# Performance work log

Hardware: AMD Instinct MI355X
Metric: run time of the kernel (lower is better)

The kernel has to match this reference:

```python
import jax, jax.numpy as jnp
import numpy as np
import math

D_MODEL = 1024
N_HEAD = 16
D_K = D_MODEL // N_HEAD  # 64
SEQ = 1024
BATCH = 8


def setup_inputs() -> dict:
    k = jax.random.key(0)
    ks = jax.random.split(k, 11)
    f32 = jnp.float32
    scale = 1.0 / math.sqrt(D_MODEL)
    return {
        "query": jax.random.normal(ks[0], (BATCH, SEQ, D_MODEL), dtype=f32),
        "key": jax.random.normal(ks[1], (BATCH, SEQ, D_MODEL), dtype=f32),
        "value": jax.random.normal(ks[2], (BATCH, SEQ, D_MODEL), dtype=f32),
        # Shaw-style relative position table a[q_pos, k_pos, d_k]
        "rel": jax.random.normal(ks[3], (SEQ, SEQ, D_K), dtype=f32) * 0.02,
        "W_q": jax.random.normal(ks[4], (D_MODEL, D_MODEL), dtype=f32) * scale,
        "b_q": jnp.zeros((D_MODEL,), dtype=f32),
        "W_k": jax.random.normal(ks[5], (D_MODEL, D_MODEL), dtype=f32) * scale,
        "b_k": jnp.zeros((D_MODEL,), dtype=f32),
        "W_v": jax.random.normal(ks[6], (D_MODEL, D_MODEL), dtype=f32) * scale,
        "b_v": jnp.zeros((D_MODEL,), dtype=f32),
        # boolean mask: True = masked out (matches torch masked_fill semantics)
        "mask": jax.random.randint(ks[7], (BATCH, SEQ, SEQ), 0, 4) == 0,
    }


def reference(query, key, value, rel, W_q, b_q, W_k, b_k, W_v, b_v, mask):
    B, S, D = query.shape
    H, dk = N_HEAD, D // N_HEAD

    def proj(x, W, b):
        # [B,S,D] -> [B,H,S,dk]
        return (x @ W + b).reshape(B, S, H, dk).transpose(0, 2, 1, 3)

    Q = proj(query, W_q, b_q)
    K = proj(key, W_k, b_k)
    V = proj(value, W_v, b_v)

    # E_1 = Q K^T / sqrt(d_k): [B,H,Sq,Sk]
    scores = jnp.einsum("bhqd,bhkd->bhqk", Q, K) / math.sqrt(dk)
    # E_2 = Q x relative_position (per query position), added UNscaled as in source
    scores = scores + jnp.einsum("bhqd,qkd->bhqk", Q, rel)
    # masked_fill(mask, -1e8)
    scores = jnp.where(mask[:, None, :, :], jnp.float32(-1e8), scores)
    attn = jax.nn.softmax(scores, axis=-1)
    out = jnp.einsum("bhqk,bhkd->bhqd", attn, V)  # [B,H,S,dk]
    return out.transpose(0, 2, 1, 3).reshape(B, S, D)
```

## Files before the change

kernel.cpp:

```cpp
#include <hip/hip_runtime.h>

typedef _Float16 h8_t __attribute__((ext_vector_type(8)));
typedef _Float16 h4_t __attribute__((ext_vector_type(4)));
typedef float f4_t __attribute__((ext_vector_type(4)));

#define MFMA16(a, b, c) __builtin_amdgcn_mfma_f32_16x16x32_f16((a), (b), (c), 0, 0, 0)

__device__ inline void gl_lds16(const _Float16* g, _Float16* l) {
    __builtin_amdgcn_global_load_lds(
        (const __attribute__((address_space(1))) unsigned int*)g,
        (__attribute__((address_space(3))) unsigned int*)l, 16, 0, 0);
}

__global__ void cvt4(const float* __restrict__ in, _Float16* __restrict__ out, int n4) {
    int i = blockIdx.x * 256 + threadIdx.x;
    if (i < n4) {
        f4_t v = *(const f4_t*)(in + (size_t)i * 4);
        h4_t h;
        for (int j = 0; j < 4; ++j) h[j] = (_Float16)v[j];
        *(h4_t*)(out + (size_t)i * 4) = h;
    }
}

__global__ void wtrans(const float* __restrict__ W, _Float16* __restrict__ Wt) {
    __shared__ float tile[32][33];
    int tid = threadIdx.x;
    int tx = tid & 31, ty = tid >> 5;
    int nb = blockIdx.x * 32, kb = blockIdx.y * 32;
    for (int p = 0; p < 4; ++p)
        tile[ty + p * 8][tx] = W[(size_t)(kb + ty + p * 8) * 1024 + nb + tx];
    __syncthreads();
    for (int p = 0; p < 4; ++p)
        Wt[(size_t)(nb + ty + p * 8) * 1024 + kb + tx] = (_Float16)tile[tx][ty + p * 8];
}

__global__ __launch_bounds__(256, 2) void proj_gemm(
    const _Float16* __restrict__ X, const _Float16* __restrict__ Wt,
    const float* __restrict__ bias, _Float16* __restrict__ Out,
    float scale, int vmode)
{
    __shared__ __align__(16) _Float16 Asm[128 * 32];
    __shared__ __align__(16) _Float16 Bsm[128 * 32];
    int tid = threadIdx.x;
    int wave = tid >> 6, lane = tid & 63;
    int l15 = lane & 15, quad = lane >> 4;
    int m0 = blockIdx.x * 128, n0 = blockIdx.y * 128;
    int wm = (wave >> 1) * 64, wn = (wave & 1) * 64;
    f4_t acc[4][4] = {};
    int f0 = wave * 128 + lane;

    for (int kt = 0; kt < 1024; kt += 32) {
        for (int j = 0; j < 2; ++j) {
            int f = f0 + j * 64;
            int r = f >> 2, c = (f & 3) * 8;
            gl_lds16(&X[(size_t)(m0 + r) * 1024 + kt + c], &Asm[f * 8]);
            gl_lds16(&Wt[(size_t)(n0 + r) * 1024 + kt + c], &Bsm[f * 8]);
        }
        __syncthreads();
        h8_t af[4], bf[4];
        for (int i = 0; i < 4; ++i) af[i] = *(const h8_t*)&Asm[(wm + i * 16 + l15) * 32 + quad * 8];
        for (int j = 0; j < 4; ++j) bf[j] = *(const h8_t*)&Bsm[(wn + j * 16 + l15) * 32 + quad * 8];
        for (int i = 0; i < 4; ++i)
            for (int j = 0; j < 4; ++j)
                acc[i][j] = MFMA16(af[i], bf[j], acc[i][j]);
        __syncthreads();
    }
    for (int j = 0; j < 4; ++j) {
        int n = n0 + wn + j * 16 + l15;
        float bv = bias[n];
        int h = n >> 6, d = n & 63;
        for (int i = 0; i < 4; ++i) {
            for (int r = 0; r < 4; ++r) {
                int m = m0 + wm + i * 16 + quad * 4 + r;
                int bb = m >> 10, ss = m & 1023;
                float v = (acc[i][j][r] + bv) * scale;
                size_t oidx = vmode ? (((size_t)(bb * 16 + h) * 64 + d) * 1024 + ss)
                                    : (((size_t)(bb * 16 + h) * 1024 + ss) * 64 + d);
                Out[oidx] = (_Float16)v;
            }
        }
    }
}

__device__ inline h8_t ld_rel(const _Float16* relh, const float* relf, size_t idx) {
    if (relh) return *(const h8_t*)(relh + idx);
    f4_t a = *(const f4_t*)(relf + idx);
    f4_t b = *(const f4_t*)(relf + idx + 4);
    h8_t h;
    for (int j = 0; j < 4; ++j) { h[j] = (_Float16)a[j]; h[4 + j] = (_Float16)b[j]; }
    return h;
}

__global__ __launch_bounds__(256, 2) void attn_kernel(
    const _Float16* __restrict__ Qh,
    const _Float16* __restrict__ Kh,
    const _Float16* __restrict__ Vt,
    const _Float16* __restrict__ relh,
    const float* __restrict__ relf,
    const int* __restrict__ mask,
    float* __restrict__ out)
{
    __shared__ __align__(16) _Float16 R_lds[2][16][17][36];
    __shared__ __align__(16) _Float16 P_lds[16][16][40];

    const int tid = threadIdx.x;
    const int wave = tid >> 6, lane = tid & 63;
    const int l15 = lane & 15, quad = lane >> 4;
    const int b = blockIdx.y;
    const int q0 = blockIdx.x * 16;

    h8_t bQ[4][2];
    h8_t bR[4][2];
    for (int gi = 0; gi < 4; ++gi) {
        int g = wave * 4 + gi;
        const _Float16* qp = Qh + ((size_t)(b * 16 + g) * 1024 + q0 + l15) * 64 + quad * 8;
        bQ[gi][0] = *(const h8_t*)qp;
        bQ[gi][1] = *(const h8_t*)(qp + 32);
    }
    for (int qi = 0; qi < 4; ++qi) {
        int q = q0 + wave * 4 + qi;
        const _Float16* qp = Qh + ((size_t)(b * 16 + l15) * 1024 + q) * 64 + quad * 8;
        bR[qi][0] = *(const h8_t*)qp;
        bR[qi][1] = *(const h8_t*)(qp + 32);
    }

    f4_t acc[4][4] = {};
    float mst[4], lst[4];
    for (int gi = 0; gi < 4; ++gi) { mst[gi] = -1e30f; lst[gi] = 0.0f; }

    int buf = 0;
    for (int t0 = 0; t0 < 1024; t0 += 32, buf ^= 1) {
        const int* mrow = &mask[((size_t)b * 1024 + q0 + l15) * 1024 + t0];
        int4 mk0 = *(const int4*)(mrow + quad * 4);
        int4 mk1 = *(const int4*)(mrow + 16 + quad * 4);

        h8_t relv[4][2][2];
        for (int qi = 0; qi < 4; ++qi) {
            size_t rb = ((size_t)(q0 + wave * 4 + qi) * 1024 + t0 + l15) * 64 + quad * 8;
            relv[qi][0][0] = ld_rel(relh, relf, rb);
            relv[qi][0][1] = ld_rel(relh, relf, rb + 32);
            relv[qi][1][0] = ld_rel(relh, relf, rb + 1024);
            relv[qi][1][1] = ld_rel(relh, relf, rb + 1056);
        }
        for (int qi = 0; qi < 4; ++qi) {
            for (int tm = 0; tm < 2; ++tm) {
                f4_t c = {0.f, 0.f, 0.f, 0.f};
                c = MFMA16(relv[qi][tm][0], bR[qi][0], c);
                c = MFMA16(relv[qi][tm][1], bR[qi][1], c);
                h4_t h;
                for (int r = 0; r < 4; ++r) h[r] = (_Float16)c[r];
                *(h4_t*)&R_lds[buf][wave * 4 + qi][l15][tm * 16 + quad * 4] = h;
            }
        }

        h8_t kv[4][2][2];
        for (int gi = 0; gi < 4; ++gi) {
            const _Float16* kp =
                Kh + ((size_t)(b * 16 + wave * 4 + gi) * 1024 + t0 + l15) * 64 + quad * 8;
            kv[gi][0][0] = *(const h8_t*)kp;
            kv[gi][0][1] = *(const h8_t*)(kp + 32);
            kv[gi][1][0] = *(const h8_t*)(kp + 1024);
            kv[gi][1][1] = *(const h8_t*)(kp + 1056);
        }
        __syncthreads();

        int mm[8] = {mk0.x, mk0.y, mk0.z, mk0.w, mk1.x, mk1.y, mk1.z, mk1.w};

        for (int gi = 0; gi < 4; ++gi) {
            int g = wave * 4 + gi;
            f4_t s[2];
            for (int tm = 0; tm < 2; ++tm) {
                h4_t rh = *(const h4_t*)&R_lds[buf][l15][g][tm * 16 + quad * 4];
                f4_t c;
                for (int r = 0; r < 4; ++r) c[r] = (float)rh[r];
                c = MFMA16(kv[gi][tm][0], bQ[gi][0], c);
                c = MFMA16(kv[gi][tm][1], bQ[gi][1], c);
                s[tm] = c;
            }
            for (int tm = 0; tm < 2; ++tm)
                for (int r = 0; r < 4; ++r)
                    if (mm[tm * 4 + r]) s[tm][r] = -1e8f;

            float mx = s[0][0];
            for (int tm = 0; tm < 2; ++tm)
                for (int r = 0; r < 4; ++r) mx = fmaxf(mx, s[tm][r]);
            mx = fmaxf(mx, __shfl_xor(mx, 16));
            mx = fmaxf(mx, __shfl_xor(mx, 32));
            float mnew = fmaxf(mst[gi], mx);
            float alpha = __expf(mst[gi] - mnew);
            mst[gi] = mnew;
            float rs = 0.0f;
            for (int tm = 0; tm < 2; ++tm)
                for (int r = 0; r < 4; ++r) {
                    float p = __expf(s[tm][r] - mnew);
                    s[tm][r] = p;
                    rs += p;
                }
            rs += __shfl_xor(rs, 16);
            rs += __shfl_xor(rs, 32);
            lst[gi] = lst[gi] * alpha + rs;
            for (int dm = 0; dm < 4; ++dm) acc[gi][dm] *= alpha;
            for (int tm = 0; tm < 2; ++tm) {
                h4_t h;
                for (int r = 0; r < 4; ++r) h[r] = (_Float16)s[tm][r];
                *(h4_t*)&P_lds[g][l15][tm * 16 + quad * 4] = h;
            }
        }

        h8_t vv[4][4];
        for (int gi = 0; gi < 4; ++gi) {
            const _Float16* vp =
                Vt + (size_t)(b * 16 + wave * 4 + gi) * 65536 + t0 + quad * 8;
            for (int dm = 0; dm < 4; ++dm)
                vv[gi][dm] = *(const h8_t*)(vp + (size_t)(dm * 16 + l15) * 1024);
        }
        for (int gi = 0; gi < 4; ++gi) {
            h8_t bp = *(const h8_t*)&P_lds[wave * 4 + gi][l15][quad * 8];
            for (int dm = 0; dm < 4; ++dm)
                acc[gi][dm] = MFMA16(vv[gi][dm], bp, acc[gi][dm]);
        }
    }

    for (int gi = 0; gi < 4; ++gi) {
        int g = wave * 4 + gi;
        float linv = 1.0f / lst[gi];
        for (int dm = 0; dm < 4; ++dm) {
            f4_t v = acc[gi][dm] * linv;
            float* op = out + ((size_t)b * 1024 + q0 + l15) * 1024 + g * 64 + dm * 16 + quad * 4;
            *(f4_t*)op = v;
        }
    }
}

extern "C" void kernel_launch(void* const* d_in, const int* in_sizes, int n_in,
                              void* d_out, int out_size, void* d_ws, size_t ws_size,
                              hipStream_t stream) {
    const float* q    = (const float*)d_in[0];
    const float* k    = (const float*)d_in[1];
    const float* v    = (const float*)d_in[2];
    const float* rel  = (const float*)d_in[3];
    const float* Wq   = (const float*)d_in[4];
    const float* bq   = (const float*)d_in[5];
    const float* Wk   = (const float*)d_in[6];
    const float* bk   = (const float*)d_in[7];
    const float* Wv   = (const float*)d_in[8];
    const float* bv   = (const float*)d_in[9];
    const int*   mask = (const int*)d_in[10];
    float* out = (float*)d_out;

    const size_t NEL = 8ull * 1024 * 1024;
    const size_t WEL = 1024ull * 1024;
    const size_t RELE = 1024ull * 1024 * 64;

    char* w = (char*)d_ws;
    size_t off = 0;
    auto alloc = [&](size_t bytes) { char* p = w + off; off += bytes; return p; };
    _Float16* qx  = (_Float16*)alloc(NEL * 2);
    _Float16* kx  = (_Float16*)alloc(NEL * 2);
    _Float16* vx  = (_Float16*)alloc(NEL * 2);
    _Float16* Wqt = (_Float16*)alloc(WEL * 2);
    _Float16* Wkt = (_Float16*)alloc(WEL * 2);
    _Float16* Wvt = (_Float16*)alloc(WEL * 2);
    _Float16* Qh  = (_Float16*)alloc(NEL * 2);
    _Float16* Kh  = (_Float16*)alloc(NEL * 2);
    _Float16* Vth = (_Float16*)alloc(NEL * 2);
    _Float16* relh = nullptr;
    if (ws_size >= off + RELE * 2) relh = (_Float16*)alloc(RELE * 2);

    cvt4<<<(int)(NEL / 4 / 256), 256, 0, stream>>>(q, qx, (int)(NEL / 4));
    cvt4<<<(int)(NEL / 4 / 256), 256, 0, stream>>>(k, kx, (int)(NEL / 4));
    cvt4<<<(int)(NEL / 4 / 256), 256, 0, stream>>>(v, vx, (int)(NEL / 4));
    if (relh)
        cvt4<<<(int)(RELE / 4 / 256), 256, 0, stream>>>(rel, relh, (int)(RELE / 4));

    dim3 tg(32, 32);
    wtrans<<<tg, 256, 0, stream>>>(Wq, Wqt);
    wtrans<<<tg, 256, 0, stream>>>(Wk, Wkt);
    wtrans<<<tg, 256, 0, stream>>>(Wv, Wvt);

    dim3 pg(64, 8);
    proj_gemm<<<pg, 256, 0, stream>>>(qx, Wqt, bq, Qh, 1.0f, 0);
    proj_gemm<<<pg, 256, 0, stream>>>(kx, Wkt, bk, Kh, 0.125f, 0);
    proj_gemm<<<pg, 256, 0, stream>>>(vx, Wvt, bv, Vth, 1.0f, 1);

    dim3 ag(64, 8);
    attn_kernel<<<ag, 256, 0, stream>>>(Qh, Kh, Vth, relh, rel, mask, out);
}
```

Baseline: 940.0 us.

## Split attention over key halves, fuse input fp16 conversion into projection GEMM

The attention kernel now splits the key dimension in two across gridDim.z. Each half writes an unnormalized partial output plus running max and sum, and a new combine kernel merges the halves. The separate fp32-to-fp16 conversion kernels for the inputs and the rel table are removed: the projection GEMM converts X while loading it, and attention always converts rel from fp32 on the fly. Other changes are a single-buffered R_lds with an added trailing barrier, occupancy launch bounds raised to 4, and many loops unrolled. The aim is more blocks in flight and fewer passes over memory. The cost is extra partial-output traffic, a combine pass, and rel being read in fp32, which is twice the bytes.

```diff
diff --git a/kernel.cpp b/kernel.cpp
--- a/kernel.cpp
+++ b/kernel.cpp
@@ -10,16 +10,6 @@
     __builtin_amdgcn_global_load_lds(
         (const __attribute__((address_space(1))) unsigned int*)g,
         (__attribute__((address_space(3))) unsigned int*)l, 16, 0, 0);
-}
-
-__global__ void cvt4(const float* __restrict__ in, _Float16* __restrict__ out, int n4) {
-    int i = blockIdx.x * 256 + threadIdx.x;
-    if (i < n4) {
-        f4_t v = *(const f4_t*)(in + (size_t)i * 4);
-        h4_t h;
-        for (int j = 0; j < 4; ++j) h[j] = (_Float16)v[j];
-        *(h4_t*)(out + (size_t)i * 4) = h;
-    }
 }
 
 __global__ void wtrans(const float* __restrict__ W, _Float16* __restrict__ Wt) {
@@ -35,7 +25,7 @@
 }
 
 __global__ __launch_bounds__(256, 2) void proj_gemm(
-    const _Float16* __restrict__ X, const _Float16* __restrict__ Wt,
+    const float* __restrict__ X, const _Float16* __restrict__ Wt,
     const float* __restrict__ bias, _Float16* __restrict__ Out,
     float scale, int vmode)
 {
@@ -50,26 +40,45 @@
     int f0 = wave * 128 + lane;
 
     for (int kt = 0; kt < 1024; kt += 32) {
+        #pragma unroll
         for (int j = 0; j < 2; ++j) {
             int f = f0 + j * 64;
             int r = f >> 2, c = (f & 3) * 8;
-            gl_lds16(&X[(size_t)(m0 + r) * 1024 + kt + c], &Asm[f * 8]);
             gl_lds16(&Wt[(size_t)(n0 + r) * 1024 + kt + c], &Bsm[f * 8]);
+        }
+        #pragma unroll
+        for (int j = 0; j < 2; ++j) {
+            int f = f0 + j * 64;
+            int r = f >> 2, c = (f & 3) * 8;
+            const float* xp = &X[(size_t)(m0 + r) * 1024 + kt + c];
+            f4_t x0 = *(const f4_t*)xp;
+            f4_t x1 = *(const f4_t*)(xp + 4);
+            h8_t h;
+            #pragma unroll
+            for (int i = 0; i < 4; ++i) { h[i] = (_Float16)x0[i]; h[4 + i] = (_Float16)x1[i]; }
+            *(h8_t*)&Asm[f * 8] = h;
         }
         __syncthreads();
         h8_t af[4], bf[4];
+        #pragma unroll
         for (int i = 0; i < 4; ++i) af[i] = *(const h8_t*)&Asm[(wm + i * 16 + l15) * 32 + quad * 8];
+        #pragma unroll
         for (int j = 0; j < 4; ++j) bf[j] = *(const h8_t*)&Bsm[(wn + j * 16 + l15) * 32 + quad * 8];
+        #pragma unroll
         for (int i = 0; i < 4; ++i)
+            #pragma unroll
             for (int j = 0; j < 4; ++j)
                 acc[i][j] = MFMA16(af[i], bf[j], acc[i][j]);
         __syncthreads();
     }
+    #pragma unroll
     for (int j = 0; j < 4; ++j) {
         int n = n0 + wn + j * 16 + l15;
         float bv = bias[n];
         int h = n >> 6, d = n & 63;
+        #pragma unroll
         for (int i = 0; i < 4; ++i) {
+            #pragma unroll
             for (int r = 0; r < 4; ++r) {
                 int m = m0 + wm + i * 16 + quad * 4 + r;
                 int bb = m >> 10, ss = m & 1023;
@@ -82,25 +91,27 @@
     }
 }
 
-__device__ inline h8_t ld_rel(const _Float16* relh, const float* relf, size_t idx) {
-    if (relh) return *(const h8_t*)(relh + idx);
+__device__ inline h8_t ld_rel32(const float* __restrict__ relf, size_t idx) {
     f4_t a = *(const f4_t*)(relf + idx);
     f4_t b = *(const f4_t*)(relf + idx + 4);
     h8_t h;
+    #pragma unroll
     for (int j = 0; j < 4; ++j) { h[j] = (_Float16)a[j]; h[4 + j] = (_Float16)b[j]; }
     return h;
 }
 
-__global__ __launch_bounds__(256, 2) void attn_kernel(
+__global__ __launch_bounds__(256, 4) void attn_kernel(
     const _Float16* __restrict__ Qh,
     const _Float16* __restrict__ Kh,
     const _Float16* __restrict__ Vt,
-    const _Float16* __restrict__ relh,
     const float* __restrict__ relf,
     const int* __restrict__ mask,
-    float* __restrict__ out)
+    float* __restrict__ out0,
+    float* __restrict__ out1,
+    float* __restrict__ mpart,
+    float* __restrict__ lpart)
 {
-    __shared__ __align__(16) _Float16 R_lds[2][16][17][36];
+    __shared__ __align__(16) _Float16 R_lds[16][17][36];
     __shared__ __align__(16) _Float16 P_lds[16][16][40];
 
     const int tid = threadIdx.x;
@@ -108,15 +119,19 @@
     const int l15 = lane & 15, quad = lane >> 4;
     const int b = blockIdx.y;
     const int q0 = blockIdx.x * 16;
+    const int kz = blockIdx.z;
+    const int tbase = kz * 512;
 
     h8_t bQ[4][2];
     h8_t bR[4][2];
+    #pragma unroll
     for (int gi = 0; gi < 4; ++gi) {
         int g = wave * 4 + gi;
         const _Float16* qp = Qh + ((size_t)(b * 16 + g) * 1024 + q0 + l15) * 64 + quad * 8;
         bQ[gi][0] = *(const h8_t*)qp;
         bQ[gi][1] = *(const h8_t*)(qp + 32);
     }
+    #pragma unroll
     for (int qi = 0; qi < 4; ++qi) {
         int q = q0 + wave * 4 + qi;
         const _Float16* qp = Qh + ((size_t)(b * 16 + l15) * 1024 + q) * 64 + quad * 8;
@@ -126,34 +141,41 @@
 
     f4_t acc[4][4] = {};
     float mst[4], lst[4];
+    #pragma unroll
     for (int gi = 0; gi < 4; ++gi) { mst[gi] = -1e30f; lst[gi] = 0.0f; }
 
-    int buf = 0;
-    for (int t0 = 0; t0 < 1024; t0 += 32, buf ^= 1) {
+    for (int it = 0; it < 16; ++it) {
+        const int t0 = tbase + it * 32;
+
         const int* mrow = &mask[((size_t)b * 1024 + q0 + l15) * 1024 + t0];
         int4 mk0 = *(const int4*)(mrow + quad * 4);
         int4 mk1 = *(const int4*)(mrow + 16 + quad * 4);
 
         h8_t relv[4][2][2];
+        #pragma unroll
         for (int qi = 0; qi < 4; ++qi) {
             size_t rb = ((size_t)(q0 + wave * 4 + qi) * 1024 + t0 + l15) * 64 + quad * 8;
-            relv[qi][0][0] = ld_rel(relh, relf, rb);
-            relv[qi][0][1] = ld_rel(relh, relf, rb + 32);
-            relv[qi][1][0] = ld_rel(relh, relf, rb + 1024);
-            relv[qi][1][1] = ld_rel(relh, relf, rb + 1056);
-        }
+            relv[qi][0][0] = ld_rel32(relf, rb);
+            relv[qi][0][1] = ld_rel32(relf, rb + 32);
+            relv[qi][1][0] = ld_rel32(relf, rb + 1024);
+            relv[qi][1][1] = ld_rel32(relf, rb + 1056);
+        }
+        #pragma unroll
         for (int qi = 0; qi < 4; ++qi) {
+            #pragma unroll
             for (int tm = 0; tm < 2; ++tm) {
                 f4_t c = {0.f, 0.f, 0.f, 0.f};
                 c = MFMA16(relv[qi][tm][0], bR[qi][0], c);
                 c = MFMA16(relv[qi][tm][1], bR[qi][1], c);
                 h4_t h;
+                #pragma unroll
                 for (int r = 0; r < 4; ++r) h[r] = (_Float16)c[r];
-                *(h4_t*)&R_lds[buf][wave * 4 + qi][l15][tm * 16 + quad * 4] = h;
+                *(h4_t*)&R_lds[wave * 4 + qi][l15][tm * 16 + quad * 4] = h;
             }
         }
 
         h8_t kv[4][2][2];
+        #pragma unroll
         for (int gi = 0; gi < 4; ++gi) {
             const _Float16* kp =
                 Kh + ((size_t)(b * 16 + wave * 4 + gi) * 1024 + t0 + l15) * 64 + quad * 8;
@@ -166,23 +188,30 @@
 
         int mm[8] = {mk0.x, mk0.y, mk0.z, mk0.w, mk1.x, mk1.y, mk1.z, mk1.w};
 
+        #pragma unroll
         for (int gi = 0; gi < 4; ++gi) {
             int g = wave * 4 + gi;
             f4_t s[2];
+            #pragma unroll
             for (int tm = 0; tm < 2; ++tm) {
-                h4_t rh = *(const h4_t*)&R_lds[buf][l15][g][tm * 16 + quad * 4];
+                h4_t rh = *(const h4_t*)&R_lds[l15][g][tm * 16 + quad * 4];
                 f4_t c;
+                #pragma unroll
                 for (int r = 0; r < 4; ++r) c[r] = (float)rh[r];
                 c = MFMA16(kv[gi][tm][0], bQ[gi][0], c);
                 c = MFMA16(kv[gi][tm][1], bQ[gi][1], c);
                 s[tm] = c;
             }
+            #pragma unroll
             for (int tm = 0; tm < 2; ++tm)
+                #pragma unroll
                 for (int r = 0; r < 4; ++r)
                     if (mm[tm * 4 + r]) s[tm][r] = -1e8f;
 
             float mx = s[0][0];
+            #pragma unroll
             for (int tm = 0; tm < 2; ++tm)
+                #pragma unroll
                 for (int r = 0; r < 4; ++r) mx = fmaxf(mx, s[tm][r]);
             mx = fmaxf(mx, __shfl_xor(mx, 16));
             mx = fmaxf(mx, __shfl_xor(mx, 32));
@@ -190,7 +219,9 @@
             float alpha = __expf(mst[gi] - mnew);
             mst[gi] = mnew;
             float rs = 0.0f;
+            #pragma unroll
             for (int tm = 0; tm < 2; ++tm)
+                #pragma unroll
                 for (int r = 0; r < 4; ++r) {
                     float p = __expf(s[tm][r] - mnew);
                     s[tm][r] = p;
@@ -199,37 +230,73 @@
             rs += __shfl_xor(rs, 16);
             rs += __shfl_xor(rs, 32);
             lst[gi] = lst[gi] * alpha + rs;
+            #pragma unroll
             for (int dm = 0; dm < 4; ++dm) acc[gi][dm] *= alpha;
+            #pragma unroll
             for (int tm = 0; tm < 2; ++tm) {
                 h4_t h;
+                #pragma unroll
                 for (int r = 0; r < 4; ++r) h[r] = (_Float16)s[tm][r];
                 *(h4_t*)&P_lds[g][l15][tm * 16 + quad * 4] = h;
             }
         }
 
         h8_t vv[4][4];
+        #pragma unroll
         for (int gi = 0; gi < 4; ++gi) {
             const _Float16* vp =
                 Vt + (size_t)(b * 16 + wave * 4 + gi) * 65536 + t0 + quad * 8;
+            #pragma unroll
             for (int dm = 0; dm < 4; ++dm)
                 vv[gi][dm] = *(const h8_t*)(vp + (size_t)(dm * 16 + l15) * 1024);
         }
+        #pragma unroll
         for (int gi = 0; gi < 4; ++gi) {
             h8_t bp = *(const h8_t*)&P_lds[wave * 4 + gi][l15][quad * 8];
+            #pragma unroll
             for (int dm = 0; dm < 4; ++dm)
                 acc[gi][dm] = MFMA16(vv[gi][dm], bp, acc[gi][dm]);
         }
-    }
-
+        __syncthreads();
+    }
+
+    float* op = kz ? out1 : out0;
+    #pragma unroll
     for (int gi = 0; gi < 4; ++gi) {
         int g = wave * 4 + gi;
-        float linv = 1.0f / lst[gi];
+        #pragma unroll
         for (int dm = 0; dm < 4; ++dm) {
-            f4_t v = acc[gi][dm] * linv;
-            float* op = out + ((size_t)b * 1024 + q0 + l15) * 1024 + g * 64 + dm * 16 + quad * 4;
-            *(f4_t*)op = v;
-        }
-    }
+            float* p = op + ((size_t)b * 1024 + q0 + l15) * 1024 + g * 64 + dm * 16 + quad * 4;
+            *(f4_t*)p = acc[gi][dm];
+        }
+        if (quad == 0) {
+            size_t mi = (((size_t)kz * 8 + b) * 16 + g) * 1024 + q0 + l15;
+            mpart[mi] = mst[gi];
+            lpart[mi] = lst[gi];
+        }
+    }
+}
+
+__global__ void combine_kernel(const float* __restrict__ part1,
+                               const float* __restrict__ mpart,
+                               const float* __restrict__ lpart,
+                               float* __restrict__ out, int n4) {
+    int i = blockIdx.x * 256 + threadIdx.x;
+    if (i >= n4) return;
+    const int ZS = 8 * 16 * 1024;
+    int h = (i >> 4) & 15;
+    int q = (i >> 8) & 1023;
+    int b = i >> 18;
+    size_t mi = ((size_t)b * 16 + h) * 1024 + q;
+    float m0 = mpart[mi], l0 = lpart[mi];
+    float m1 = mpart[mi + ZS], l1 = lpart[mi + ZS];
+    float M = fmaxf(m0, m1);
+    float w0 = __expf(m0 - M), w1 = __expf(m1 - M);
+    float inv = 1.0f / (l0 * w0 + l1 * w1);
+    f4_t o0 = *(const f4_t*)(out + (size_t)i * 4);
+    f4_t o1 = *(const f4_t*)(part1 + (size_t)i * 4);
+    f4_t r = (o0 * w0 + o1 * w1) * inv;
+    *(f4_t*)(out + (size_t)i * 4) = r;
 }
 
 extern "C" void kernel_launch(void* const* d_in, const int* in_sizes, int n_in,
@@ -250,28 +317,19 @@
 
     const size_t NEL = 8ull * 1024 * 1024;
     const size_t WEL = 1024ull * 1024;
-    const size_t RELE = 1024ull * 1024 * 64;
 
     char* w = (char*)d_ws;
     size_t off = 0;
     auto alloc = [&](size_t bytes) { char* p = w + off; off += bytes; return p; };
-    _Float16* qx  = (_Float16*)alloc(NEL * 2);
-    _Float16* kx  = (_Float16*)alloc(NEL * 2);
-    _Float16* vx  = (_Float16*)alloc(NEL * 2);
     _Float16* Wqt = (_Float16*)alloc(WEL * 2);
     _Float16* Wkt = (_Float16*)alloc(WEL * 2);
     _Float16* Wvt = (_Float16*)alloc(WEL * 2);
     _Float16* Qh  = (_Float16*)alloc(NEL * 2);
     _Float16* Kh  = (_Float16*)alloc(NEL * 2);
     _Float16* Vth = (_Float16*)alloc(NEL * 2);
-    _Float16* relh = nullptr;
-    if (ws_size >= off + RELE * 2) relh = (_Float16*)alloc(RELE * 2);
-
-    cvt4<<<(int)(NEL / 4 / 256), 256, 0, stream>>>(q, qx, (int)(NEL / 4));
-    cvt4<<<(int)(NEL / 4 / 256), 256, 0, stream>>>(k, kx, (int)(NEL / 4));
-    cvt4<<<(int)(NEL / 4 / 256), 256, 0, stream>>>(v, vx, (int)(NEL / 4));
-    if (relh)
-        cvt4<<<(int)(RELE / 4 / 256), 256, 0, stream>>>(rel, relh, (int)(RELE / 4));
+    float* part1 = (float*)alloc(NEL * 4);
+    float* mpart = (float*)alloc(2ull * 8 * 16 * 1024 * 4);
+    float* lpart = (float*)alloc(2ull * 8 * 16 * 1024 * 4);
 
     dim3 tg(32, 32);
     wtrans<<<tg, 256, 0, stream>>>(Wq, Wqt);
@@ -279,10 +337,13 @@
     wtrans<<<tg, 256, 0, stream>>>(Wv, Wvt);
 
     dim3 pg(64, 8);
-    proj_gemm<<<pg, 256, 0, stream>>>(qx, Wqt, bq, Qh, 1.0f, 0);
-    proj_gemm<<<pg, 256, 0, stream>>>(kx, Wkt, bk, Kh, 0.125f, 0);
-    proj_gemm<<<pg, 256, 0, stream>>>(vx, Wvt, bv, Vth, 1.0f, 1);
-
-    dim3 ag(64, 8);
-    attn_kernel<<<ag, 256, 0, stream>>>(Qh, Kh, Vth, relh, rel, mask, out);
-}
+    proj_gemm<<<pg, 256, 0, stream>>>(q, Wqt, bq, Qh, 1.0f, 0);
+    proj_gemm<<<pg, 256, 0, stream>>>(k, Wkt, bk, Kh, 0.125f, 0);
+    proj_gemm<<<pg, 256, 0, stream>>>(v, Wvt, bv, Vth, 1.0f, 1);
+
+    dim3 ag(64, 8, 2);
+    attn_kernel<<<ag, 256, 0, stream>>>(Qh, Kh, Vth, rel, mask, out, part1, mpart, lpart);
+
+    int n4 = (int)(NEL / 4);
+    combine_kernel<<<(n4 + 255) / 256, 256, 0, stream>>>(part1, mpart, lpart, out, n4);
+}
```

After: 1.341 ms. +42.6%, slower.
